# Performance work log

Measured on AMD Instinct MI355X. Metric: run time of the kernel, lower is better.

## Reference

```python
import jax, jax.numpy as jnp
import numpy as np

NUM_ITEMS = 100000
NUM_ENTITIES = 1000000
EMBED_DIM = 64
BATCH = 16384
NUM_NEIGHBORS = 50


def setup_inputs() -> dict:
    key = jax.random.key(0)
    k1, k2, k3, k4, k5, k6 = jax.random.split(key, 6)
    item_indices = jax.random.randint(k1, (BATCH,), 0, NUM_ITEMS, dtype=jnp.int32)
    neighbor_indices = jax.random.randint(k2, (BATCH, NUM_NEIGHBORS), 0, NUM_ENTITIES, dtype=jnp.int32)
    item_table = jax.random.normal(k3, (NUM_ITEMS, EMBED_DIM), dtype=jnp.float32)
    entity_table = jax.random.normal(k4, (NUM_ENTITIES, EMBED_DIM), dtype=jnp.float32)
    # nn.Linear default init scale ~ 1/sqrt(fan_in)
    W = jax.random.uniform(k5, (EMBED_DIM, EMBED_DIM), dtype=jnp.float32, minval=-1.0, maxval=1.0) / jnp.sqrt(EMBED_DIM)
    b = jax.random.uniform(k6, (EMBED_DIM,), dtype=jnp.float32, minval=-1.0, maxval=1.0) / jnp.sqrt(EMBED_DIM)
    return {
        "item_indices": item_indices,
        "neighbor_indices": neighbor_indices,
        "item_table": item_table,
        "entity_table": entity_table,
        "W": W,
        "b": b,
    }


def reference(item_indices, neighbor_indices, item_table, entity_table, W, b):
    # [B, D] item embedding gather
    item_emb = item_table[item_indices]
    # [B, K, D] neighbor gather -> mean over K
    neighbor_emb = entity_table[neighbor_indices].mean(axis=1)
    x = item_emb + neighbor_emb
    # Linear + ReLU (dropout is identity in eval mode)
    x = jax.nn.relu(x @ W.T + b)
    return x
```

## Files before the change

### kernel.cpp

```cpp
#include <hip/hip_runtime.h>

#define NUM_ITEMS 100000
#define NUM_ENTITIES 1000000
#define EMBED_DIM 64
#define BATCH 16384
#define NUM_NEIGHBORS 50

#define RPB 16
#define THREADS 256

__global__ __launch_bounds__(THREADS) void kgat_fused_kernel(
    const int* __restrict__ item_idx,
    const int* __restrict__ nbr_idx,
    const float* __restrict__ item_tab,
    const float* __restrict__ ent_tab,
    const float* __restrict__ W,
    const float* __restrict__ bias,
    float* __restrict__ out)
{
    __shared__ float xs[RPB][EMBED_DIM];
    __shared__ float Wl[EMBED_DIM][EMBED_DIM + 1];

    const int t    = threadIdx.x;
    const int lane = t & 63;
    const int wave = t >> 6;
    const int row0 = blockIdx.x * RPB;

    #pragma unroll
    for (int i = t; i < EMBED_DIM * EMBED_DIM; i += THREADS) {
        Wl[i >> 6][i & 63] = W[i];
    }

    {
        float acc[4] = {0.f, 0.f, 0.f, 0.f};
        const int rbase = row0 + wave * 4;

        #pragma unroll 2
        for (int k = 0; k < NUM_NEIGHBORS; ++k) {
            #pragma unroll
            for (int rr = 0; rr < 4; ++rr) {
                const int idx = nbr_idx[(rbase + rr) * NUM_NEIGHBORS + k];
                acc[rr] += ent_tab[(size_t)idx * EMBED_DIM + lane];
            }
        }

        #pragma unroll
        for (int rr = 0; rr < 4; ++rr) {
            const int it = item_idx[rbase + rr];
            float x = acc[rr] * (1.0f / NUM_NEIGHBORS)
                    + item_tab[(size_t)it * EMBED_DIM + lane];
            xs[wave * 4 + rr][lane] = x;
        }
    }

    __syncthreads();

    {
        const int j = lane;
        const int r0 = wave;
        float a0 = 0.f, a1 = 0.f, a2 = 0.f, a3 = 0.f;

        #pragma unroll
        for (int d = 0; d < EMBED_DIM; ++d) {
            const float w = Wl[j][d];
            a0 = fmaf(xs[r0     ][d], w, a0);
            a1 = fmaf(xs[r0 +  4][d], w, a1);
            a2 = fmaf(xs[r0 +  8][d], w, a2);
            a3 = fmaf(xs[r0 + 12][d], w, a3);
        }

        const float bb = bias[j];
        out[(size_t)(row0 + r0     ) * EMBED_DIM + j] = fmaxf(a0 + bb, 0.f);
        out[(size_t)(row0 + r0 +  4) * EMBED_DIM + j] = fmaxf(a1 + bb, 0.f);
        out[(size_t)(row0 + r0 +  8) * EMBED_DIM + j] = fmaxf(a2 + bb, 0.f);
        out[(size_t)(row0 + r0 + 12) * EMBED_DIM + j] = fmaxf(a3 + bb, 0.f);
    }
}

extern "C" void kernel_launch(void* const* d_in, const int* in_sizes, int n_in,
                              void* d_out, int out_size, void* d_ws, size_t ws_size,
                              hipStream_t stream) {
    const int*   item_idx = (const int*)  d_in[0];
    const int*   nbr_idx  = (const int*)  d_in[1];
    const float* item_tab = (const float*)d_in[2];
    const float* ent_tab  = (const float*)d_in[3];
    const float* W        = (const float*)d_in[4];
    const float* bias     = (const float*)d_in[5];
    float*       out      = (float*)      d_out;

    dim3 grid(BATCH / RPB);
    dim3 block(THREADS);
    kgat_fused_kernel<<<grid, block, 0, stream>>>(
        item_idx, nbr_idx, item_tab, ent_tab, W, bias, out);
}
```

Measured before the change: 41.17 us.

## Stage neighbor indices in LDS and gather embeddings with float4 loads

Neighbor and item indices for the block are now loaded cooperatively into shared memory before the gather. Each wave then covers four rows at once, with 16 lanes per row each loading a float4, in place of one float per lane across serial rows. The aim is fewer dependent index loads and wider 16-byte gathers that raise memory-level parallelism. In exchange it adds an extra barrier and more shared memory, and the unroll-by-10 loop may raise register pressure.

Result: no change. 40.92 us (-0.6%).

```diff
diff --git a/kernel.cpp b/kernel.cpp
--- a/kernel.cpp
+++ b/kernel.cpp
@@ -1,10 +1,8 @@
 #include <hip/hip_runtime.h>
 
-#define NUM_ITEMS 100000
-#define NUM_ENTITIES 1000000
 #define EMBED_DIM 64
 #define BATCH 16384
-#define NUM_NEIGHBORS 50
+#define K_NBR 50
 
 #define RPB 16
 #define THREADS 256
@@ -18,7 +16,9 @@
     const float* __restrict__ bias,
     float* __restrict__ out)
 {
-    __shared__ float xs[RPB][EMBED_DIM];
+    __shared__ int   ids[RPB * K_NBR];
+    __shared__ int   itid[RPB];
+    __shared__ float xs[RPB][EMBED_DIM + 4];
     __shared__ float Wl[EMBED_DIM][EMBED_DIM + 1];
 
     const int t    = threadIdx.x;
@@ -27,30 +27,41 @@
     const int row0 = blockIdx.x * RPB;
 
     #pragma unroll
-    for (int i = t; i < EMBED_DIM * EMBED_DIM; i += THREADS) {
+    for (int i = t; i < EMBED_DIM * EMBED_DIM; i += THREADS)
         Wl[i >> 6][i & 63] = W[i];
-    }
+    #pragma unroll
+    for (int i = t; i < RPB * K_NBR; i += THREADS)
+        ids[i] = nbr_idx[(size_t)row0 * K_NBR + i];
+    if (t < RPB) itid[t] = item_idx[row0 + t];
+    __syncthreads();
 
     {
-        float acc[4] = {0.f, 0.f, 0.f, 0.f};
-        const int rbase = row0 + wave * 4;
+        const int q = lane >> 4;
+        const int c = lane & 15;
+        const int r = wave * 4 + q;
+        const int idbase = r * K_NBR;
 
-        #pragma unroll 2
-        for (int k = 0; k < NUM_NEIGHBORS; ++k) {
-            #pragma unroll
-            for (int rr = 0; rr < 4; ++rr) {
-                const int idx = nbr_idx[(rbase + rr) * NUM_NEIGHBORS + k];
-                acc[rr] += ent_tab[(size_t)idx * EMBED_DIM + lane];
-            }
+        const float4* __restrict__ ent4  = (const float4*)ent_tab;
+        const float4* __restrict__ item4 = (const float4*)item_tab;
+
+        float4 acc = make_float4(0.f, 0.f, 0.f, 0.f);
+
+        #pragma unroll 10
+        for (int k = 0; k < K_NBR; ++k) {
+            const int idx = ids[idbase + k];
+            const float4 v = ent4[(size_t)idx * (EMBED_DIM / 4) + c];
+            acc.x += v.x; acc.y += v.y; acc.z += v.z; acc.w += v.w;
         }
 
-        #pragma unroll
-        for (int rr = 0; rr < 4; ++rr) {
-            const int it = item_idx[rbase + rr];
-            float x = acc[rr] * (1.0f / NUM_NEIGHBORS)
-                    + item_tab[(size_t)it * EMBED_DIM + lane];
-            xs[wave * 4 + rr][lane] = x;
-        }
+        const int it = itid[r];
+        const float4 iv = item4[(size_t)it * (EMBED_DIM / 4) + c];
+        const float s = 1.0f / K_NBR;
+        float4 x;
+        x.x = fmaf(acc.x, s, iv.x);
+        x.y = fmaf(acc.y, s, iv.y);
+        x.z = fmaf(acc.z, s, iv.z);
+        x.w = fmaf(acc.w, s, iv.w);
+        *(float4*)&xs[r][c * 4] = x;
     }
 
     __syncthreads();
```
